# Optimization experiments

Hardware: AMD Instinct MI355X
Metric: run time of the kernel (lower is better)

Reference implementation:

```python
import jax, jax.numpy as jnp
import numpy as np

N_CAMS = 6
N_RAYS = 200
N_UNI = 32
N_G = 4
N_PG = 8
MAX_D = 100.0
SOM_SIG = 2.0
GRID_W = 400
RAW_W, RAW_H = 1600.0, 900.0
SCENE = np.array([-51.2, -51.2, -5.0, 51.2, 51.2, 3.0], dtype=np.float32)
LOSS_W = {'kl': 1.0, 'dist2closest': 0.01, 'color': 1.0, 'reprojection': 1.0}


def _pe(x):
    freqs = jnp.pi * (2.0 ** jnp.arange(6, dtype=x.dtype))
    xb = x[..., None, :] * freqs[:, None]
    flat = lambda t: t.reshape(t.shape[:-2] + (t.shape[-2] * t.shape[-1],))
    return jnp.concatenate([x, flat(jnp.sin(xb)), flat(jnp.cos(xb))], axis=-1)


def _bilinear(img, u, v):
    C, H, W = img.shape
    x0 = jnp.floor(u)
    y0 = jnp.floor(v)
    valid = (u >= 0) & (u <= W - 1) & (v >= 0) & (v <= H - 1)
    x0i = jnp.clip(x0.astype(jnp.int32), 0, W - 1)
    x1i = jnp.clip(x0i + 1, 0, W - 1)
    y0i = jnp.clip(y0.astype(jnp.int32), 0, H - 1)
    y1i = jnp.clip(y0i + 1, 0, H - 1)
    wx = u - x0
    wy = v - y0
    out = (img[:, y0i, x0i] * ((1 - wx) * (1 - wy))[None]
           + img[:, y0i, x1i] * (wx * (1 - wy))[None]
           + img[:, y1i, x0i] * ((1 - wx) * wy)[None]
           + img[:, y1i, x1i] * (wx * wy)[None])
    out = jnp.moveaxis(out, 0, -1) * valid[..., None]
    return out, valid


def _resnet_fc(feat, z, win, bin_, wz, bz, w0, b0, w1, b1, wout, bout):
    x = feat @ win + bin_
    for i in range(wz.shape[0]):
        x = x + z @ wz[i] + bz[i]
        h = jax.nn.relu(x)
        h = jax.nn.relu(h @ w0[i] + b0[i])
        h = h @ w1[i] + b1[i]
        x = x + h
    return jax.nn.relu(x) @ wout + bout


def _forward(cam_feat, bev_feat, source_imgs, target_imgs, raw_cam_Ks, source_cam_Ks,
             lidar2cams, source_cam2input_lidars, source_cam2target_cams,
             mlp_win, mlp_bin, mlp_wz, mlp_bz, mlp_w0, mlp_b0, mlp_w1, mlp_b1, mlp_wout, mlp_bout,
             g_win, g_bin, g_wz, g_bz, g_w0, g_b0, g_w1, g_b1, g_wout, g_bout, pixel_idx):
    cf = cam_feat[0]
    bf = bev_feat[0]
    si = source_imgs[0, 0]
    ti = target_imgs[0, 0]
    rK = raw_cam_Ks[0, :, :3, :3]
    sK = source_cam_Ks[0, 0, :, :3, :3]
    invK = jnp.linalg.inv(sK)
    l2c = lidar2cams[0]
    s2in = source_cam2input_lidars[0, 0]
    s2tg = source_cam2target_cams[0, 0]
    center = jnp.asarray((SCENE[:3] + SCENE[3:]) / 2.0)
    half = jnp.asarray((SCENE[3:] - SCENE[:3]) / 2.0)
    mlp_p = (mlp_win, mlp_bin, mlp_wz, mlp_bz, mlp_w0, mlp_b0, mlp_w1, mlp_b1, mlp_wout, mlp_bout)
    g_p = (g_win, g_bin, g_wz, g_bz, g_w0, g_b0, g_w1, g_b1, g_wout, g_bout)

    def per_cam(cf_c, si_c, ti_c, rK_c, sK_c, invK_c, l2c_c, s2in_c, s2tg_c, idx):
        N = idx.shape[0]
        x = (idx % GRID_W).astype(jnp.float32) * 2.0
        y = (idx // GRID_W).astype(jnp.float32) * 2.0
        pix_h = jnp.stack([x, y, jnp.ones_like(x)], axis=-1)
        dirs = pix_h @ invK_c.T
        d_u = (jnp.arange(N_UNI, dtype=jnp.float32) + 0.5) / N_UNI * MAX_D
        d_u_b = jnp.broadcast_to(d_u, (N, N_UNI))
        Hf, Wf = cf_c.shape[1], cf_c.shape[2]
        Hb, Wb = bf.shape[1], bf.shape[2]

        def eval_pts(d):
            pts_cam = dirs[:, None, :] * d[..., None]
            pts_lid = pts_cam @ s2in_c[:3, :3].T + s2in_c[:3, 3]
            pc = pts_lid @ l2c_c[:3, :3].T + l2c_c[:3, 3]
            z = pc[..., 2]
            zs = jnp.maximum(z, 1e-3)
            uvw = pc @ rK_c.T
            fu = uvw[..., 0] / zs * (Wf / RAW_W)
            fv = uvw[..., 1] / zs * (Hf / RAW_H)
            cam_lat, cval = _bilinear(cf_c, fu, fv)
            cval = cval & (z > 0.1)
            bx = (pts_lid[..., 0] - SCENE[0]) / (SCENE[3] - SCENE[0]) * (Wb - 1)
            by = (pts_lid[..., 1] - SCENE[1]) / (SCENE[4] - SCENE[1]) * (Hb - 1)
            bev_lat, bval = _bilinear(bf, bx, by)
            valid = cval & bval
            latent = jnp.concatenate([bev_lat, cam_lat], axis=-1) * valid[..., None]
            pln = (pts_lid - center) / half
            pcn = pts_cam / MAX_D
            vd = dirs / jnp.linalg.norm(dirs, axis=-1, keepdims=True)
            vdl = vd @ s2in_c[:3, :3].T
            vd_b = jnp.broadcast_to(vd[:, None, :], pcn.shape)
            vdl_b = jnp.broadcast_to(vdl[:, None, :], pcn.shape)
            feat = jnp.concatenate([_pe(pln), vdl_b, _pe(pcn), vd_b], axis=-1)
            return feat, latent, valid

        featc, latc, _valc = eval_pts(d_u_b)
        g = _resnet_fc(featc, latc, *g_p)
        logits = g[..., 0].reshape(N, N_G, N_PG)
        sval = g[..., 1].reshape(N, N_G, N_PG)
        wg = jax.nn.softmax(logits, axis=-1)
        d_grp = d_u.reshape(N_G, N_PG)
        mu = jnp.sum(wg * d_grp, axis=-1)
        std = jax.nn.softplus(jnp.sum(wg * sval, axis=-1)) + 0.1
        offs = jnp.linspace(-2.0, 2.0, N_PG)
        d_g = jnp.clip(mu[..., None] + std[..., None] * offs, 0.5, MAX_D).reshape(N, N_G * N_PG)
        d_all = jnp.sort(jnp.concatenate([d_u_b, d_g], axis=-1), axis=-1)

        featf, latf, valf = eval_pts(d_all)
        out = _resnet_fc(featf, latf, *mlp_p)
        rgb = jax.nn.sigmoid(out[..., :3])
        vf = valf.astype(jnp.float32)
        sigma = jax.nn.softplus(out[..., 3]) * vf
        delta = jnp.concatenate([d_all[..., 1:] - d_all[..., :-1],
                                 jnp.full((N, 1), 1e3, jnp.float32)], axis=-1)
        alpha = 1.0 - jnp.exp(-sigma * delta)
        trans = jnp.cumprod(1.0 - alpha + 1e-10, axis=-1)
        trans = jnp.concatenate([jnp.ones((N, 1), jnp.float32), trans[..., :-1]], axis=-1)
        w = alpha * trans
        color = jnp.sum(w[..., None] * rgb, axis=-2)
        depth = jnp.sum(w * d_all, axis=-1)
        rvr = vf.mean(axis=-1)

        dist2 = (d_all[:, None, :] - mu[:, :, None]) ** 2
        resp = jax.nn.softmax(-dist2 / (2.0 * SOM_SIG ** 2), axis=1)
        rw = resp * w[:, None, :] + 1e-8
        som_mean = jnp.sum(rw * d_all[:, None, :], axis=-1) / jnp.sum(rw, axis=-1)
        som_var = jnp.sum(rw * (d_all[:, None, :] - som_mean[..., None]) ** 2, axis=-1) / jnp.sum(rw, axis=-1)
        som_std = jnp.sqrt(som_var + 1e-6)
        kl = jnp.log(som_std / std) + (std ** 2 + (mu - som_mean) ** 2) / (2.0 * (som_var + 1e-6)) - 0.5
        loss_kl = kl.mean()

        dg = jnp.abs(mu - jax.lax.stop_gradient(depth)[:, None])
        loss_d2c = dg.min(axis=-1).mean()

        csrc, _ = _bilinear(si_c, x, y)
        loss_color = (jnp.abs(csrc - color) * rvr[:, None]).mean()

        pts_c = dirs * depth[:, None]
        pts_t = pts_c @ s2tg_c[:3, :3].T + s2tg_c[:3, 3]
        zt = jnp.maximum(pts_t[..., 2], 1e-3)
        uvt = pts_t @ sK_c.T
        pred, tval = _bilinear(ti_c, uvt[..., 0] / zt, uvt[..., 1] / zt)
        mask = (tval & (pts_t[..., 2] > 0.1) & (depth < 30.0)).astype(jnp.float32)
        l1 = jnp.abs(pred - csrc).mean(axis=-1)
        loss_re = jnp.sum(l1 * mask) / (jnp.sum(mask) + 1e-6)
        return loss_color, loss_kl, loss_d2c, loss_re

    lc, lkl, ld, lr = jax.vmap(per_cam)(cf, si, ti, rK, sK, invK, l2c, s2in, s2tg, pixel_idx)
    lr = jnp.where(jnp.isnan(lr), 0.0, lr)
    denom = float(N_CAMS)
    total = (LOSS_W['color'] * lc.sum() + LOSS_W['kl'] * lkl.sum()
             + LOSS_W['dist2closest'] * ld.sum() + LOSS_W['reprojection'] * lr.sum()) / denom
    return total


def setup_inputs() -> dict:
    key = jax.random.key(0)
    ks = jax.random.split(key, 8)
    f32 = jnp.float32
    cam_feat = jax.random.normal(ks[0], (1, 6, 256, 56, 100), f32)
    bev_feat = jax.random.normal(ks[1], (1, 512, 200, 200), f32)
    source_imgs = jax.random.uniform(ks[2], (1, 1, 6, 3, 300, 800), f32)
    target_imgs = jax.random.uniform(ks[3], (1, 1, 6, 3, 300, 800), f32)
    pixel_idx = jax.random.randint(ks[4], (6, N_RAYS), 0, GRID_W * 150)

    def rz(a):
        c, s = np.cos(a), np.sin(a)
        return np.array([[c, -s, 0.0], [s, c, 0.0], [0.0, 0.0, 1.0]], dtype=np.float32)
    A = np.array([[0, -1, 0], [0, 0, -1], [1, 0, 0]], dtype=np.float32)
    l2c = np.zeros((6, 4, 4), np.float32)
    for i in range(6):
        l2c[i, :3, :3] = A @ rz(-i * np.pi / 3)
        l2c[i, :3, 3] = np.array([0.0, 0.8, 0.5], np.float32)
        l2c[i, 3, 3] = 1.0
    s2in = np.linalg.inv(l2c).astype(np.float32)
    s2in[:, 0, 3] += 0.3
    s2tg = np.tile(np.eye(4, dtype=np.float32), (6, 1, 1))
    ang = 0.03
    s2tg[:, 0, 0] = np.cos(ang); s2tg[:, 0, 2] = np.sin(ang)
    s2tg[:, 2, 0] = -np.sin(ang); s2tg[:, 2, 2] = np.cos(ang)
    s2tg[:, 0, 3] = 0.3; s2tg[:, 2, 3] = 0.1
    rK = np.tile(np.eye(4, dtype=np.float32), (6, 1, 1))
    rK[:, 0, 0] = 800.0; rK[:, 1, 1] = 800.0; rK[:, 0, 2] = 800.0; rK[:, 1, 2] = 450.0
    sKm = np.tile(np.eye(4, dtype=np.float32), (6, 1, 1))
    sKm[:, 0, 0] = 400.0; sKm[:, 1, 1] = 400.0; sKm[:, 0, 2] = 400.0; sKm[:, 1, 2] = 150.0

    D_IN, D_H, D_LAT, NB = 84, 512, 768, 3

    def mk(k, dout):
        kk = jax.random.split(k, 5)
        return dict(
            win=jax.random.normal(kk[0], (D_IN, D_H), f32) * 0.1,
            bin=jnp.zeros((D_H,), f32),
            wz=jax.random.normal(kk[1], (NB, D_LAT, D_H), f32) * 0.036,
            bz=jnp.zeros((NB, D_H), f32),
            w0=jax.random.normal(kk[2], (NB, D_H, D_H), f32) * 0.044,
            b0=jnp.zeros((NB, D_H), f32),
            w1=jax.random.normal(kk[3], (NB, D_H, D_H), f32) * 0.044,
            b1=jnp.zeros((NB, D_H), f32),
            wout=jax.random.normal(kk[4], (D_H, dout), f32) * 0.044,
            bout=jnp.zeros((dout,), f32),
        )
    mp = mk(ks[5], 4)
    gp = mk(ks[6], 2)
    inp = {
        'cam_feat': cam_feat, 'bev_feat': bev_feat,
        'source_imgs': source_imgs, 'target_imgs': target_imgs,
        'raw_cam_Ks': jnp.asarray(rK)[None],
        'source_cam_Ks': jnp.asarray(sKm)[None, None],
        'lidar2cams': jnp.asarray(l2c)[None],
        'source_cam2input_lidars': jnp.asarray(s2in)[None, None],
        'source_cam2target_cams': jnp.asarray(s2tg)[None, None],
        'pixel_idx': pixel_idx,
    }
    for n, v in mp.items():
        inp['mlp_' + n] = v
    for n, v in gp.items():
        inp['g_' + n] = v
    return inp


def reference(cam_feat, bev_feat, source_imgs, target_imgs, raw_cam_Ks, source_cam_Ks,
              lidar2cams, source_cam2input_lidars, source_cam2target_cams,
              mlp_win, mlp_bin, mlp_wz, mlp_bz, mlp_w0, mlp_b0, mlp_w1, mlp_b1, mlp_wout, mlp_bout,
              g_win, g_bin, g_wz, g_bz, g_w0, g_b0, g_w1, g_b1, g_wout, g_bout, pixel_idx):
    return _forward(cam_feat, bev_feat, source_imgs, target_imgs, raw_cam_Ks, source_cam_Ks,
                    lidar2cams, source_cam2input_lidars, source_cam2target_cams,
                    mlp_win, mlp_bin, mlp_wz, mlp_bz, mlp_w0, mlp_b0, mlp_w1, mlp_b1, mlp_wout, mlp_bout,
                    g_win, g_bin, g_wz, g_bz, g_w0, g_b0, g_w1, g_b1, g_wout, g_bout, pixel_idx)
```

## Files before the change

### kernel.cpp

```cpp
#include <hip/hip_runtime.h>
#include <math.h>

typedef unsigned int uint32;
typedef short bf16x8 __attribute__((ext_vector_type(8)));
typedef float f32x4 __attribute__((ext_vector_type(4)));

__device__ __forceinline__ float sigmoidf_(float x){ return 1.0f/(1.0f+expf(-x)); }
__device__ __forceinline__ float softplusf_(float x){ return x>20.0f ? x : log1pf(expf(x)); }
__device__ __forceinline__ int iclampi(int v,int lo,int hi){ return v<lo?lo:(v>hi?hi:v); }

__device__ __forceinline__ float bf2f(uint32 u){ return __uint_as_float(u<<16); }
__device__ __forceinline__ unsigned short f2bf(float f){
  uint32 x = __float_as_uint(f);
  uint32 r = (x + 0x7fffu + ((x>>16)&1u)) >> 16;
  return (unsigned short)r;
}

typedef __attribute__((address_space(1))) const unsigned int ga_u32;
typedef __attribute__((address_space(3))) unsigned int ls_u32;
__device__ __forceinline__ void gl_lds16(const unsigned short* g, unsigned short* l){
  __builtin_amdgcn_global_load_lds((ga_u32*)g, (ls_u32*)l, 16, 0, 0);
}

__device__ __forceinline__ float pe_elem(int s, float vx, float vy, float vz){
  const float F0 = 3.14159265358979f;
  if (s < 3) return s==0?vx:(s==1?vy:vz);
  s -= 3;
  bool isCos = false;
  if (s >= 18){ s -= 18; isCos = true; }
  int fi = s/3, ci = s%3;
  float v = ci==0?vx:(ci==1?vy:vz);
  float f = F0 * (float)(1<<fi);
  return isCos ? cosf(f*v) : sinf(f*v);
}

__global__ __launch_bounds__(256) void transpose_cb_k(const float* __restrict__ in,
    unsigned short* __restrict__ out, int C, int S, int Cout,
    size_t inStride, size_t outStride, int rowStride)
{
  __shared__ float tile[32][33];
  int b = blockIdx.z;
  int s0 = blockIdx.x*32, c0 = blockIdx.y*32;
  int tx = threadIdx.x & 31, ty = threadIdx.x >> 5;
  #pragma unroll
  for (int i=0;i<32;i+=8){
    int c = c0+ty+i, s = s0+tx;
    tile[ty+i][tx] = (c<C && s<S) ? in[(size_t)b*inStride + (size_t)c*S + s] : 0.0f;
  }
  __syncthreads();
  #pragma unroll
  for (int i=0;i<32;i+=8){
    int s = s0+ty+i, c = c0+tx;
    if (s<S && c<Cout) out[(size_t)b*outStride + (size_t)s*rowStride + c] = f2bf(tile[tx][ty+i]);
  }
}

__global__ void combine_bias_k(const float* __restrict__ m_b1, const float* __restrict__ m_bz,
                               const float* __restrict__ g_b1, const float* __restrict__ g_bz,
                               float* __restrict__ CB)
{
  int idx = blockIdx.x*blockDim.x + threadIdx.x;
  if (idx >= 2048) return;
  int w = idx >> 9, n = idx & 511;
  const float* b1 = (w < 2) ? m_b1 : g_b1;
  const float* bz = (w < 2) ? m_bz : g_bz;
  int i = w & 1;
  CB[idx] = b1[i*512 + n] + bz[(i+1)*512 + n];
}

__global__ void setup_rays_k(const int* __restrict__ pix, const float* __restrict__ sK_all,
                             const float* __restrict__ s2in_all,
                             float* __restrict__ dirs, float* __restrict__ vd,
                             float* __restrict__ vdl)
{
  int r = blockIdx.x*blockDim.x + threadIdx.x;
  if (r >= 1200) return;
  int cam = r / 200;
  const float* sK = sK_all + cam*16;
  const float* s2in = s2in_all + cam*16;
  float a=sK[0],b=sK[1],c=sK[2],d=sK[4],e=sK[5],f=sK[6],g=sK[8],h=sK[9],i=sK[10];
  float det = a*(e*i-f*h) - b*(d*i-f*g) + c*(d*h-e*g);
  float inv00=(e*i-f*h)/det, inv01=(c*h-b*i)/det, inv02=(b*f-c*e)/det;
  float inv10=(f*g-d*i)/det, inv11=(a*i-c*g)/det, inv12=(c*d-a*f)/det;
  float inv20=(d*h-e*g)/det, inv21=(b*g-a*h)/det, inv22=(a*e-b*d)/det;
  int idx = pix[r];
  float x = (float)(idx % 400) * 2.0f;
  float y = (float)(idx / 400) * 2.0f;
  float dx = inv00*x + inv01*y + inv02;
  float dy = inv10*x + inv11*y + inv12;
  float dz = inv20*x + inv21*y + inv22;
  dirs[r*3+0]=dx; dirs[r*3+1]=dy; dirs[r*3+2]=dz;
  float n = sqrtf(dx*dx+dy*dy+dz*dz);
  float vx=dx/n, vy=dy/n, vz=dz/n;
  vd[r*3+0]=vx; vd[r*3+1]=vy; vd[r*3+2]=vz;
  vdl[r*3+0]=s2in[0]*vx + s2in[1]*vy + s2in[2]*vz;
  vdl[r*3+1]=s2in[4]*vx + s2in[5]*vy + s2in[6]*vz;
  vdl[r*3+2]=s2in[8]*vx + s2in[9]*vy + s2in[10]*vz;
}

__global__ __launch_bounds__(256) void eval2_k(
    const unsigned short* __restrict__ camT,
    const unsigned short* __restrict__ bevT,
    const float* __restrict__ dirs, const float* __restrict__ vd, const float* __restrict__ vdl,
    const float* __restrict__ dall, int ndepth, int R0,
    const float* __restrict__ s2in_all, const float* __restrict__ l2c_all, const float* __restrict__ rK_all,
    unsigned short* __restrict__ feat, unsigned short* __restrict__ cat, float* __restrict__ vf)
{
  int p  = blockIdx.x;
  int rl = p / ndepth;
  int j  = p - rl*ndepth;
  int R  = R0 + rl;
  int cam = R / 200;
  const float* s2in = s2in_all + cam*16;
  const float* l2c  = l2c_all + cam*16;
  const float* rK   = rK_all + cam*16;
  float dx = dirs[R*3+0], dy = dirs[R*3+1], dz = dirs[R*3+2];
  float d = dall ? dall[(size_t)rl*ndepth + j] : (((float)j + 0.5f)/32.0f)*100.0f;
  float px = dx*d, py = dy*d, pz = dz*d;
  float lx = s2in[0]*px + s2in[1]*py + s2in[2]*pz + s2in[3];
  float ly = s2in[4]*px + s2in[5]*py + s2in[6]*pz + s2in[7];
  float lz = s2in[8]*px + s2in[9]*py + s2in[10]*pz + s2in[11];
  float ccx = l2c[0]*lx + l2c[1]*ly + l2c[2]*lz + l2c[3];
  float ccy = l2c[4]*lx + l2c[5]*ly + l2c[6]*lz + l2c[7];
  float ccz = l2c[8]*lx + l2c[9]*ly + l2c[10]*lz + l2c[11];
  float zs = fmaxf(ccz, 0.001f);
  float uu = rK[0]*ccx + rK[1]*ccy + rK[2]*ccz;
  float vv = rK[4]*ccx + rK[5]*ccy + rK[6]*ccz;
  float fu = uu/zs*(100.0f/1600.0f);
  float fv = vv/zs*(56.0f/900.0f);
  bool cvalid = (fu>=0.0f)&&(fu<=99.0f)&&(fv>=0.0f)&&(fv<=55.0f)&&(ccz>0.1f);
  float cfx0 = floorf(fu), cfy0 = floorf(fv);
  int cx0=iclampi((int)cfx0,0,99), cx1=iclampi(cx0+1,0,99);
  int cy0=iclampi((int)cfy0,0,55), cy1=iclampi(cy0+1,0,55);
  float cwx=fu-cfx0, cwy=fv-cfy0;
  float cw00=(1-cwx)*(1-cwy), cw01=cwx*(1-cwy), cw10=(1-cwx)*cwy, cw11=cwx*cwy;
  float bx = (lx+51.2f)/102.4f*199.0f;
  float by = (ly+51.2f)/102.4f*199.0f;
  bool bvalid = (bx>=0.0f)&&(bx<=199.0f)&&(by>=0.0f)&&(by<=199.0f);
  float bfx0=floorf(bx), bfy0=floorf(by);
  int bx0=iclampi((int)bfx0,0,199), bx1=iclampi(bx0+1,0,199);
  int by0=iclampi((int)bfy0,0,199), by1=iclampi(by0+1,0,199);
  float bwx=bx-bfx0, bwy=by-bfy0;
  float bw00=(1-bwx)*(1-bwy), bw01=bwx*(1-bwy), bw10=(1-bwx)*bwy, bw11=bwx*bwy;
  float vflag = (cvalid && bvalid) ? 1.0f : 0.0f;
  int t = threadIdx.x;
  uint32* catrow = (uint32*)(cat + (size_t)p*1280);
  {
    size_t sb00 = (size_t)(by0*200+bx0)*512, sb01 = (size_t)(by0*200+bx1)*512;
    size_t sb10 = (size_t)(by1*200+bx0)*512, sb11 = (size_t)(by1*200+bx1)*512;
    uint32 u00 = ((const uint32*)(bevT + sb00))[t];
    uint32 u01 = ((const uint32*)(bevT + sb01))[t];
    uint32 u10 = ((const uint32*)(bevT + sb10))[t];
    uint32 u11 = ((const uint32*)(bevT + sb11))[t];
    float lo = bw00*bf2f(u00&0xffffu) + bw01*bf2f(u01&0xffffu) + bw10*bf2f(u10&0xffffu) + bw11*bf2f(u11&0xffffu);
    float hi = bw00*bf2f(u00>>16) + bw01*bf2f(u01>>16) + bw10*bf2f(u10>>16) + bw11*bf2f(u11>>16);
    lo *= vflag; hi *= vflag;
    catrow[256 + t] = (uint32)f2bf(lo) | ((uint32)f2bf(hi)<<16);
  }
  if (t < 128){
    const unsigned short* cfT = camT + (size_t)cam*5600*256;
    size_t sc00 = (size_t)(cy0*100+cx0)*256, sc01 = (size_t)(cy0*100+cx1)*256;
    size_t sc10 = (size_t)(cy1*100+cx0)*256, sc11 = (size_t)(cy1*100+cx1)*256;
    uint32 u00 = ((const uint32*)(cfT + sc00))[t];
    uint32 u01 = ((const uint32*)(cfT + sc01))[t];
    uint32 u10 = ((const uint32*)(cfT + sc10))[t];
    uint32 u11 = ((const uint32*)(cfT + sc11))[t];
    float lo = cw00*bf2f(u00&0xffffu) + cw01*bf2f(u01&0xffffu) + cw10*bf2f(u10&0xffffu) + cw11*bf2f(u11&0xffffu);
    float hi = cw00*bf2f(u00>>16) + cw01*bf2f(u01>>16) + cw10*bf2f(u10>>16) + cw11*bf2f(u11>>16);
    lo *= vflag; hi *= vflag;
    catrow[512 + t] = (uint32)f2bf(lo) | ((uint32)f2bf(hi)<<16);
  }
  if (t < 128){
    float val = 0.0f;
    if (t < 84){
      float plx = lx/51.2f, ply = ly/51.2f, plz = (lz+1.0f)/4.0f;
      float pcx = px/100.0f, pcy = py/100.0f, pcz = pz/100.0f;
      float vx=vd[R*3], vy=vd[R*3+1], vz=vd[R*3+2];
      float wx=vdl[R*3], wy=vdl[R*3+1], wz=vdl[R*3+2];
      if (t < 39)      val = pe_elem(t, plx, ply, plz);
      else if (t < 42) val = (t==39)?wx:((t==40)?wy:wz);
      else if (t < 81) val = pe_elem(t-42, pcx, pcy, pcz);
      else             val = (t==81)?vx:((t==82)?vy:vz);
    }
    feat[(size_t)p*128 + t] = f2bf(val);
  }
  if (vf && t==0) vf[p] = vflag;
}

#define GBM 128
#define GBN 128
#define GBK 64
template<int ACC, int RELU_OUT, int WRITE_XR>
__global__ __launch_bounds__(256) void mgemm_k(
    const unsigned short* __restrict__ A, int lda,
    const unsigned short* __restrict__ BT,
    const float* __restrict__ bias,
    unsigned short* __restrict__ C, int ldc,
    unsigned short* __restrict__ XR,
    int M, int N, int K)
{
  __shared__ unsigned short As[GBM*GBK];
  __shared__ unsigned short Bs[GBN*GBK];
  int w = blockIdx.x;
  int xcd = w & 7, ii = w >> 3;
  int colp = ii & 3, rgrp = ii >> 2;
  int rowp = rgrp*8 + xcd;
  int row0 = rowp*GBM, col0 = colp*GBN;
  if (row0 >= M) return;
  int tid = threadIdx.x;
  int lane = tid & 63, wave = tid >> 6;
  int wm = wave >> 1, wn = wave & 1;
  int l15 = lane & 15, l4 = lane >> 4;
  int lrow = lane >> 3;
  int lch  = lane & 7;
  int chsw = (lch ^ lrow) * 8;
  const unsigned short* aptr = A  + (size_t)(row0 + wave*32 + lrow)*lda + chsw;
  const unsigned short* bptr = BT + (size_t)(col0 + wave*32 + lrow)*K   + chsw;
  unsigned short* asl = &As[(wave*32)*64];
  unsigned short* bsl = &Bs[(wave*32)*64];

  f32x4 acc[4][4];
  #pragma unroll
  for (int mi=0;mi<4;++mi)
    #pragma unroll
    for (int nj=0;nj<4;++nj){ f32x4 z = {0.f,0.f,0.f,0.f}; acc[mi][nj] = z; }

  for (int k0 = 0; k0 < K; k0 += GBK){
    #pragma unroll
    for (int i=0;i<4;++i) gl_lds16(aptr + (size_t)i*8*lda + k0, asl + i*8*64);
    #pragma unroll
    for (int i=0;i<4;++i) gl_lds16(bptr + (size_t)i*8*K   + k0, bsl + i*8*64);
    __syncthreads();
    #pragma unroll
    for (int ks=0; ks<2; ++ks){
      bf16x8 a[4], b[4];
      #pragma unroll
      for (int mi=0;mi<4;++mi){
        int row = wm*64 + mi*16 + l15;
        int sc = (ks*4 + l4) ^ (row&7);
        a[mi] = *(const bf16x8*)&As[row*64 + sc*8];
      }
      #pragma unroll
      for (int nj=0;nj<4;++nj){
        int colr = wn*64 + nj*16 + l15;
        int sc = (ks*4 + l4) ^ (colr&7);
        b[nj] = *(const bf16x8*)&Bs[colr*64 + sc*8];
      }
      #pragma unroll
      for (int mi=0;mi<4;++mi)
        #pragma unroll
        for (int nj=0;nj<4;++nj)
          acc[mi][nj] = __builtin_amdgcn_mfma_f32_16x16x32_bf16(a[mi], b[nj], acc[mi][nj], 0,0,0);
    }
    __syncthreads();
  }
  #pragma unroll
  for (int mi=0;mi<4;++mi){
    int gr0 = row0 + wm*64 + mi*16 + l4*4;
    #pragma unroll
    for (int nj=0;nj<4;++nj){
      int gc = col0 + wn*64 + nj*16 + l15;
      if (gc >= N) continue;
      float bv = bias[gc];
      #pragma unroll
      for (int i=0;i<4;++i){
        int gr = gr0 + i;
        if (gr >= M) continue;
        float v = acc[mi][nj][i] + bv;
        if (ACC) v += bf2f((uint32)C[(size_t)gr*ldc + gc]);
        if (RELU_OUT) v = fmaxf(v, 0.0f);
        C[(size_t)gr*ldc + gc] = f2bf(v);
        if (WRITE_XR) XR[(size_t)gr*512 + gc] = f2bf(fmaxf(v, 0.0f));
      }
    }
  }
}

static inline int gemm_grid(int M){
  int nrow = (M + GBM - 1)/GBM;
  int nrowp = (nrow + 7) & ~7;
  return nrowp * 4;
}

__global__ __launch_bounds__(256) void outlayer_w_k(const unsigned short* __restrict__ X,
    const float* __restrict__ W, const float* __restrict__ b, float* __restrict__ O,
    int M, int dout)
{
  int wid = threadIdx.x >> 6, lane = threadIdx.x & 63;
  int row = blockIdx.x*4 + wid;
  if (row >= M) return;
  const unsigned short* xr = X + (size_t)row*512;
  float s[4] = {0,0,0,0};
  for (int k=lane; k<512; k+=64){
    float xv = fmaxf(bf2f((uint32)xr[k]), 0.0f);
    #pragma unroll
    for (int c=0;c<4;++c)
      if (c < dout) s[c] += xv * W[(size_t)k*dout + c];
  }
  #pragma unroll
  for (int c=0;c<4;++c)
    #pragma unroll
    for (int m=32;m;m>>=1) s[c] += __shfl_xor(s[c], m, 64);
  if (lane == 0)
    for (int c=0;c<dout;++c) O[(size_t)row*dout + c] = s[c] + b[c];
}

__global__ void coarse_post_k(const float* __restrict__ OUTB, float* __restrict__ MU,
                              float* __restrict__ STD, float* __restrict__ DALL,
                              int R0, int rn)
{
  int rl = blockIdx.x*blockDim.x + threadIdx.x;
  if (rl >= rn) return;
  int R = R0 + rl;
  float mu[4], sd[4];
  for (int g=0; g<4; ++g){
    float lg[8], sv[8], mx = -1e30f;
    for (int pp=0; pp<8; ++pp){
      int j = g*8+pp;
      lg[pp] = OUTB[((size_t)rl*32 + j)*2 + 0];
      sv[pp] = OUTB[((size_t)rl*32 + j)*2 + 1];
      mx = fmaxf(mx, lg[pp]);
    }
    float se = 0.0f;
    for (int pp=0; pp<8; ++pp){ lg[pp] = expf(lg[pp]-mx); se += lg[pp]; }
    float m=0.0f, s=0.0f;
    for (int pp=0; pp<8; ++pp){
      float wgt = lg[pp]/se;
      float du = (((float)(g*8+pp)+0.5f)/32.0f)*100.0f;
      m += wgt*du; s += wgt*sv[pp];
    }
    mu[g]=m; sd[g]=softplusf_(s)+0.1f;
    MU[R*4+g]=mu[g]; STD[R*4+g]=sd[g];
  }
  float da[64];
  for (int j=0;j<32;++j) da[j] = (((float)j+0.5f)/32.0f)*100.0f;
  for (int g=0; g<4; ++g)
    for (int pp=0; pp<8; ++pp){
      float off = -2.0f + (4.0f/7.0f)*(float)pp;
      float v = mu[g] + sd[g]*off;
      v = fminf(fmaxf(v, 0.5f), 100.0f);
      da[32 + g*8+pp] = v;
    }
  for (int i=1;i<64;++i){ float key=da[i]; int k=i-1;
    while (k>=0 && da[k]>key){ da[k+1]=da[k]; --k; } da[k+1]=key; }
  for (int j=0;j<64;++j) DALL[(size_t)rl*64+j] = da[j];
}

__device__ __forceinline__ void bilin_img(const float* __restrict__ img, int H, int W,
                                          float u, float v, float* out3, bool* valid)
{
  *valid = (u>=0.0f)&&(u<=(float)(W-1))&&(v>=0.0f)&&(v<=(float)(H-1));
  float fx0=floorf(u), fy0=floorf(v);
  int x0=iclampi((int)fx0,0,W-1), x1=iclampi(x0+1,0,W-1);
  int y0=iclampi((int)fy0,0,H-1), y1=iclampi(y0+1,0,H-1);
  float wx=u-fx0, wy=v-fy0;
  float w00=(1-wx)*(1-wy), w01=wx*(1-wy), w10=(1-wx)*wy, w11=wx*wy;
  for (int ch=0; ch<3; ++ch){
    const float* p = img + (size_t)ch*H*W;
    out3[ch] = w00*p[y0*W+x0] + w01*p[y0*W+x1] + w10*p[y1*W+x0] + w11*p[y1*W+x1];
  }
}

__global__ __launch_bounds__(256) void render_loss_w_k(
  const float* __restrict__ OUTB, const float* __restrict__ VF,
  const float* __restrict__ DALL, const float* __restrict__ MU, const float* __restrict__ STD,
  const float* __restrict__ dirs, const int* __restrict__ pix,
  const float* __restrict__ src_imgs, const float* __restrict__ tgt_imgs,
  const float* __restrict__ s2tg_all, const float* __restrict__ sK_all,
  float* __restrict__ acc, int R0, int rn)
{
  int wid = threadIdx.x >> 6, lane = threadIdx.x & 63;
  int rl = blockIdx.x*4 + wid;
  if (rl >= rn) return;
  int R = R0 + rl;
  int cam = R / 200;
  int j = lane;
  float dj = DALL[(size_t)rl*64 + j];
  float delta = (j<63) ? (DALL[(size_t)rl*64 + j + 1] - dj) : 1000.0f;
  f32x4 o = *(const f32x4*)(OUTB + ((size_t)rl*64 + j)*4);
  float vfp = VF[(size_t)rl*64 + j];
  float sg = softplusf_(o[3])*vfp;
  float alpha = 1.0f - expf(-sg*delta);
  float prod = 1.0f - alpha + 1e-10f;
  #pragma unroll
  for (int dstep=1; dstep<64; dstep<<=1){
    float v = __shfl_up(prod, dstep, 64);
    if (lane >= dstep) prod *= v;
  }
  float T = __shfl_up(prod, 1, 64);
  if (lane == 0) T = 1.0f;
  float w = alpha*T;
  float c0 = w*sigmoidf_(o[0]), c1 = w*sigmoidf_(o[1]), c2 = w*sigmoidf_(o[2]);
  float dsum = w*dj, vs = vfp;
  #pragma unroll
  for (int m=32;m;m>>=1){
    c0 += __shfl_xor(c0,m,64); c1 += __shfl_xor(c1,m,64); c2 += __shfl_xor(c2,m,64);
    dsum += __shfl_xor(dsum,m,64); vs += __shfl_xor(vs,m,64);
  }
// ... 42 lines not shown
  #pragma unroll
  for (int g=0;g<4;++g) mind = fminf(mind, fabsf(mu[g]-depth));
  const float* si = src_imgs + (size_t)cam*3*300*800;
  const float* ti = tgt_imgs + (size_t)cam*3*300*800;
  const float* s2tg = s2tg_all + cam*16;
  const float* sK = sK_all + cam*16;
  int idx = pix[R];
  float x = (float)(idx % 400) * 2.0f;
  float y = (float)(idx / 400) * 2.0f;
  float csrc[3]; bool sval;
  bilin_img(si, 300, 800, x, y, csrc, &sval);
  if (!sval){ csrc[0]=0; csrc[1]=0; csrc[2]=0; }
  float csum = fabsf(csrc[0]-c0)+fabsf(csrc[1]-c1)+fabsf(csrc[2]-c2);
  float dx=dirs[R*3], dy=dirs[R*3+1], dz=dirs[R*3+2];
  float px=dx*depth, py=dy*depth, pz=dz*depth;
  float tx=s2tg[0]*px+s2tg[1]*py+s2tg[2]*pz+s2tg[3];
  float ty=s2tg[4]*px+s2tg[5]*py+s2tg[6]*pz+s2tg[7];
  float tz=s2tg[8]*px+s2tg[9]*py+s2tg[10]*pz+s2tg[11];
  float zt=fmaxf(tz,0.001f);
  float uu=(sK[0]*tx+sK[1]*ty+sK[2]*tz)/zt;
  float vv=(sK[4]*tx+sK[5]*ty+sK[6]*tz)/zt;
  float pred[3]; bool tval;
  bilin_img(ti, 300, 800, uu, vv, pred, &tval);
  float tvf = tval?1.0f:0.0f;
  pred[0]*=tvf; pred[1]*=tvf; pred[2]*=tvf;
  float mask = (tval && (tz>0.1f) && (depth<30.0f)) ? 1.0f : 0.0f;
  float l1 = (fabsf(pred[0]-csrc[0])+fabsf(pred[1]-csrc[1])+fabsf(pred[2]-csrc[2]))*(1.0f/3.0f);
  float* a = acc + cam*8;
  atomicAdd(&a[0], csum*rvr);
  atomicAdd(&a[1], klsum);
  atomicAdd(&a[2], mind);
  atomicAdd(&a[3], l1*mask);
  atomicAdd(&a[4], mask);
}

__global__ void zero_acc_k(float* a){ a[threadIdx.x] = 0.0f; }

__global__ void finalize_k(const float* __restrict__ acc, float* __restrict__ out){
  if (threadIdx.x==0 && blockIdx.x==0){
    float tot = 0.0f;
    for (int c=0;c<6;++c){
      const float* a = acc + c*8;
      float lc  = a[0] / 600.0f;
      float lkl = a[1] / 800.0f;
      float ld  = a[2] / 200.0f;
      float lr  = a[3] / (a[4] + 1e-6f);
      if (lr != lr) lr = 0.0f;
      tot += lc + lkl + 0.01f*ld + lr;
    }
    out[0] = tot / 6.0f;
  }
}

static void run_mlp4(hipStream_t stream, int M,
   const unsigned short* WinT, const float* bin,
   const unsigned short* WzT,  const float* bz,
   const unsigned short* W0T,  const float* b0,
   const unsigned short* W1Wz, const float* CB,
   const unsigned short* W1T2, const float* b1,
   const float* wout, const float* bout, int dout,
   const unsigned short* FEAT, unsigned short* CAT,
   unsigned short* X, unsigned short* XR, float* OUTB)
{
  int g = gemm_grid(M);
  mgemm_k<0,0,1><<<g,256,0,stream>>>(FEAT, 128, WinT, bin, X, 512, XR, M, 512, 128);
  mgemm_k<1,0,1><<<g,256,0,stream>>>(CAT+512, 1280, WzT, bz, X, 512, XR, M, 512, 768);
  for (int i=0;i<2;++i){
    mgemm_k<0,1,0><<<g,256,0,stream>>>(XR, 512, W0T + (size_t)i*512*512, b0 + i*512, CAT, 1280, nullptr, M, 512, 512);
    mgemm_k<1,0,1><<<g,256,0,stream>>>(CAT, 1280, W1Wz + (size_t)i*512*1280, CB + i*512, X, 512, XR, M, 512, 1280);
  }
  mgemm_k<0,1,0><<<g,256,0,stream>>>(XR, 512, W0T + (size_t)2*512*512, b0 + 2*512, CAT, 1280, nullptr, M, 512, 512);
  mgemm_k<1,0,0><<<g,256,0,stream>>>(CAT, 1280, W1T2, b1 + 2*512, X, 512, nullptr, M, 512, 512);
  outlayer_w_k<<<(M+3)/4, 256, 0, stream>>>(X, wout, bout, OUTB, M, dout);
}

extern "C" void kernel_launch(void* const* d_in, const int* in_sizes, int n_in,
                              void* d_out, int out_size, void* d_ws, size_t ws_size,
                              hipStream_t stream) {
  (void)in_sizes; (void)n_in; (void)out_size;
  const float* cam_feat = (const float*)d_in[0];
  const float* bev_feat = (const float*)d_in[1];
  const float* src_imgs = (const float*)d_in[2];
  const float* tgt_imgs = (const float*)d_in[3];
  const float* rK   = (const float*)d_in[4];
  const float* sK   = (const float*)d_in[5];
  const float* l2c  = (const float*)d_in[6];
  const float* s2in = (const float*)d_in[7];
  const float* s2tg = (const float*)d_in[8];
  const int*   pix  = (const int*)d_in[9];
  const float* mlp_win = (const float*)d_in[10];
  const float* mlp_bin = (const float*)d_in[11];
  const float* mlp_wz  = (const float*)d_in[12];
  const float* mlp_bz  = (const float*)d_in[13];
  const float* mlp_w0  = (const float*)d_in[14];
  const float* mlp_b0  = (const float*)d_in[15];
  const float* mlp_w1  = (const float*)d_in[16];
  const float* mlp_b1  = (const float*)d_in[17];
  const float* mlp_wout= (const float*)d_in[18];
  const float* mlp_bout= (const float*)d_in[19];
  const float* g_win = (const float*)d_in[20];
  const float* g_bin = (const float*)d_in[21];
  const float* g_wz  = (const float*)d_in[22];
  const float* g_bz  = (const float*)d_in[23];
  const float* g_w0  = (const float*)d_in[24];
  const float* g_b0  = (const float*)d_in[25];
  const float* g_w1  = (const float*)d_in[26];
  const float* g_b1  = (const float*)d_in[27];
  const float* g_wout= (const float*)d_in[28];
  const float* g_bout= (const float*)d_in[29];

  char* base = (char*)d_ws;
  size_t off = 0;
  auto alloc = [&](size_t bytes)->char*{
    char* p = base + off;
    off = (off + bytes + 255) & ~(size_t)255;
    return p;
  };
  float* ACC  = (float*)alloc(64*4);
  float* DIR  = (float*)alloc(3600*4);
  float* VD   = (float*)alloc(3600*4);
  float* VDL  = (float*)alloc(3600*4);
  float* MU   = (float*)alloc(4800*4);
  float* STD  = (float*)alloc(4800*4);
  float* CBm  = (float*)alloc(2048*4);
  unsigned short* bevT = (unsigned short*)alloc((size_t)40000*512*2);
  unsigned short* camT = (unsigned short*)alloc((size_t)6*5600*256*2);
  unsigned short* gWinT = (unsigned short*)alloc((size_t)512*128*2);
  unsigned short* mWinT = (unsigned short*)alloc((size_t)512*128*2);
  unsigned short* gWzT  = (unsigned short*)alloc((size_t)512*768*2);
  unsigned short* mWzT  = (unsigned short*)alloc((size_t)512*768*2);
  unsigned short* gW0T  = (unsigned short*)alloc((size_t)3*512*512*2);
  unsigned short* mW0T  = (unsigned short*)alloc((size_t)3*512*512*2);
  unsigned short* gW1Wz = (unsigned short*)alloc((size_t)2*512*1280*2);
  unsigned short* mW1Wz = (unsigned short*)alloc((size_t)2*512*1280*2);
  unsigned short* gW1T2 = (unsigned short*)alloc((size_t)512*512*2);
  unsigned short* mW1T2 = (unsigned short*)alloc((size_t)512*512*2);
  size_t fixed = off;
  const size_t perray = 256 + 16384 + 163840 + 65536 + 65536 + 1024 + 256;
  const size_t SLACK = 512*1024;
  int Rc = 1200;
  {
    size_t need = fixed + (size_t)1200*perray + SLACK + 8192;
    if (need > ws_size){
      size_t avail = (ws_size > fixed + SLACK + 8192) ? (ws_size - fixed - SLACK - 8192) : perray;
      Rc = (int)(avail / perray);
      if (Rc < 1) Rc = 1;
      if (Rc > 1200) Rc = 1200;
    }
  }
  float*          DALL = (float*)alloc((size_t)Rc*64*4);
  unsigned short* FEAT = (unsigned short*)alloc((size_t)Rc*64*128*2);
  unsigned short* CAT  = (unsigned short*)alloc((size_t)Rc*64*1280*2);
  unsigned short* X    = (unsigned short*)alloc((size_t)Rc*64*512*2);
  unsigned short* XR   = (unsigned short*)alloc((size_t)Rc*64*512*2);
  float*          OUTB = (float*)alloc((size_t)Rc*64*4*4);
  float*          VF   = (float*)alloc((size_t)Rc*64*4);

  { dim3 g((40000+31)/32, (512+31)/32, 1);
    transpose_cb_k<<<g,256,0,stream>>>(bev_feat, bevT, 512, 40000, 512, 0, 0, 512); }
  { dim3 g((5600+31)/32, (256+31)/32, 6);
    transpose_cb_k<<<g,256,0,stream>>>(cam_feat, camT, 256, 5600, 256, (size_t)256*5600, (size_t)5600*256, 256); }
  { dim3 g((512+31)/32, (128+31)/32, 1);
    transpose_cb_k<<<g,256,0,stream>>>(g_win,  gWinT, 84, 512, 128, 0, 0, 128);
    transpose_cb_k<<<g,256,0,stream>>>(mlp_win, mWinT, 84, 512, 128, 0, 0, 128); }
  { dim3 g((512+31)/32, (768+31)/32, 1);
    transpose_cb_k<<<g,256,0,stream>>>(g_wz,  gWzT, 768, 512, 768, 0, 0, 768);
    transpose_cb_k<<<g,256,0,stream>>>(mlp_wz, mWzT, 768, 512, 768, 0, 0, 768); }
  { dim3 g((512+31)/32, (512+31)/32, 3);
    transpose_cb_k<<<g,256,0,stream>>>(g_w0,  gW0T, 512, 512, 512, (size_t)512*512, (size_t)512*512, 512);
    transpose_cb_k<<<g,256,0,stream>>>(mlp_w0, mW0T, 512, 512, 512, (size_t)512*512, (size_t)512*512, 512); }
  { dim3 g((512+31)/32, (512+31)/32, 2);
    transpose_cb_k<<<g,256,0,stream>>>(g_w1,  gW1Wz, 512, 512, 512, (size_t)512*512, (size_t)512*1280, 1280);
    transpose_cb_k<<<g,256,0,stream>>>(mlp_w1, mW1Wz, 512, 512, 512, (size_t)512*512, (size_t)512*1280, 1280); }
  { dim3 g((512+31)/32, (768+31)/32, 2);
    transpose_cb_k<<<g,256,0,stream>>>(g_wz + (size_t)768*512,  gW1Wz + 512, 768, 512, 768, (size_t)768*512, (size_t)512*1280, 1280);
    transpose_cb_k<<<g,256,0,stream>>>(mlp_wz + (size_t)768*512, mW1Wz + 512, 768, 512, 768, (size_t)768*512, (size_t)512*1280, 1280); }
  { dim3 g((512+31)/32, (512+31)/32, 1);
    transpose_cb_k<<<g,256,0,stream>>>(g_w1 + (size_t)2*512*512,  gW1T2, 512, 512, 512, 0, 0, 512);
    transpose_cb_k<<<g,256,0,stream>>>(mlp_w1 + (size_t)2*512*512, mW1T2, 512, 512, 512, 0, 0, 512); }
  combine_bias_k<<<8,256,0,stream>>>(mlp_b1, mlp_bz, g_b1, g_bz, CBm);

  zero_acc_k<<<1,64,0,stream>>>(ACC);
  setup_rays_k<<<5,256,0,stream>>>(pix, sK, s2in, DIR, VD, VDL);

  for (int R0=0; R0<1200; R0+=Rc){
    int rn = (1200 - R0 < Rc) ? (1200 - R0) : Rc;
    int Pc = rn*32;
    eval2_k<<<Pc,256,0,stream>>>(camT, bevT, DIR, VD, VDL,
        nullptr, 32, R0, s2in, l2c, rK, FEAT, CAT, nullptr);
    run_mlp4(stream, Pc, gWinT,g_bin, gWzT,g_bz, gW0T,g_b0, gW1Wz, CBm+1024,
             gW1T2, g_b1, g_wout, g_bout, 2, FEAT, CAT, X, XR, OUTB);
    coarse_post_k<<<(rn+255)/256,256,0,stream>>>(OUTB, MU, STD, DALL, R0, rn);
    int Pf = rn*64;
    eval2_k<<<Pf,256,0,stream>>>(camT, bevT, DIR, VD, VDL,
        DALL, 64, R0, s2in, l2c, rK, FEAT, CAT, VF);
    run_mlp4(stream, Pf, mWinT,mlp_bin, mWzT,mlp_bz, mW0T,mlp_b0, mW1Wz, CBm,
             mW1T2, mlp_b1, mlp_wout, mlp_bout, 4, FEAT, CAT, X, XR, OUTB);
    render_loss_w_k<<<(rn+3)/4,256,0,stream>>>(OUTB, VF, DALL, MU, STD,
        DIR, pix, src_imgs, tgt_imgs, s2tg, sK, ACC, R0, rn);
  }
  finalize_k<<<1,1,0,stream>>>(ACC, (float*)d_out);
}
```

Baseline: 2.463 ms.

## Fuse input and latent GEMMs, double-buffer GEMM LDS, parallelize coarse post

The positional-encoding features now go straight into an extra slice of the concatenated row buffer, so the input projection (K=128) and the latent projection (K=768) become a single K=896 GEMM with pre-combined biases. This drops one GEMM launch and the separate FEAT buffer per MLP call. The GEMM kernel double-buffers its LDS tiles so the next tile's global-to-LDS load overlaps the MFMAs, removing one barrier per k-step at the cost of twice the shared memory. The per-ray coarse post-processing now runs one wavefront per ray, using shuffle reductions and a rank-based sort in place of a serial per-thread insertion sort.

```diff
diff --git a/kernel.cpp b/kernel.cpp
--- a/kernel.cpp
+++ b/kernel.cpp
@@ -57,15 +57,21 @@
 
 __global__ void combine_bias_k(const float* __restrict__ m_b1, const float* __restrict__ m_bz,
                                const float* __restrict__ g_b1, const float* __restrict__ g_bz,
+                               const float* __restrict__ m_bin, const float* __restrict__ g_bin,
                                float* __restrict__ CB)
 {
   int idx = blockIdx.x*blockDim.x + threadIdx.x;
-  if (idx >= 2048) return;
+  if (idx >= 3072) return;
   int w = idx >> 9, n = idx & 511;
-  const float* b1 = (w < 2) ? m_b1 : g_b1;
-  const float* bz = (w < 2) ? m_bz : g_bz;
-  int i = w & 1;
-  CB[idx] = b1[i*512 + n] + bz[(i+1)*512 + n];
+  float v;
+  if (w < 4){
+    const float* b1 = (w < 2) ? m_b1 : g_b1;
+    const float* bz = (w < 2) ? m_bz : g_bz;
+    int i = w & 1;
+    v = b1[i*512 + n] + bz[(i+1)*512 + n];
+  } else if (w == 4) v = m_bin[n] + m_bz[n];
+  else               v = g_bin[n] + g_bz[n];
+  CB[idx] = v;
 }
 
 __global__ void setup_rays_k(const int* __restrict__ pix, const float* __restrict__ sK_all,
@@ -104,7 +110,7 @@
     const float* __restrict__ dirs, const float* __restrict__ vd, const float* __restrict__ vdl,
     const float* __restrict__ dall, int ndepth, int R0,
     const float* __restrict__ s2in_all, const float* __restrict__ l2c_all, const float* __restrict__ rK_all,
-    unsigned short* __restrict__ feat, unsigned short* __restrict__ cat, float* __restrict__ vf)
+    unsigned short* __restrict__ cat, float* __restrict__ vf)
 {
   int p  = blockIdx.x;
   int rl = p / ndepth;
@@ -144,7 +150,7 @@
   float bw00=(1-bwx)*(1-bwy), bw01=bwx*(1-bwy), bw10=(1-bwx)*bwy, bw11=bwx*bwy;
   float vflag = (cvalid && bvalid) ? 1.0f : 0.0f;
   int t = threadIdx.x;
-  uint32* catrow = (uint32*)(cat + (size_t)p*1280);
+  uint32* catrow = (uint32*)(cat + (size_t)p*1408);
   {
     size_t sb00 = (size_t)(by0*200+bx0)*512, sb01 = (size_t)(by0*200+bx1)*512;
     size_t sb10 = (size_t)(by1*200+bx0)*512, sb11 = (size_t)(by1*200+bx1)*512;
@@ -170,19 +176,20 @@
     lo *= vflag; hi *= vflag;
     catrow[512 + t] = (uint32)f2bf(lo) | ((uint32)f2bf(hi)<<16);
   }
-  if (t < 128){
-    float val = 0.0f;
-    if (t < 84){
-      float plx = lx/51.2f, ply = ly/51.2f, plz = (lz+1.0f)/4.0f;
-      float pcx = px/100.0f, pcy = py/100.0f, pcz = pz/100.0f;
-      float vx=vd[R*3], vy=vd[R*3+1], vz=vd[R*3+2];
-      float wx=vdl[R*3], wy=vdl[R*3+1], wz=vdl[R*3+2];
-      if (t < 39)      val = pe_elem(t, plx, ply, plz);
-      else if (t < 42) val = (t==39)?wx:((t==40)?wy:wz);
-      else if (t < 81) val = pe_elem(t-42, pcx, pcy, pcz);
-      else             val = (t==81)?vx:((t==82)?vy:vz);
-    }
-    feat[(size_t)p*128 + t] = f2bf(val);
+  if (t < 64){
+    float plx = lx/51.2f, ply = ly/51.2f, plz = (lz+1.0f)/4.0f;
+    float pcx = px/100.0f, pcy = py/100.0f, pcz = pz/100.0f;
+    float vx=vd[R*3], vy=vd[R*3+1], vz=vd[R*3+2];
+    float wx=vdl[R*3], wy=vdl[R*3+1], wz=vdl[R*3+2];
+    auto featv = [&](int s)->float{
+      if (s >= 84) return 0.0f;
+      if (s < 39)  return pe_elem(s, plx, ply, plz);
+      if (s < 42)  return (s==39)?wx:((s==40)?wy:wz);
+      if (s < 81)  return pe_elem(s-42, pcx, pcy, pcz);
+      return (s==81)?vx:((s==82)?vy:vz);
+    };
+    float v0 = featv(2*t), v1 = featv(2*t+1);
+    catrow[640 + t] = (uint32)f2bf(v0) | ((uint32)f2bf(v1)<<16);
   }
   if (vf && t==0) vf[p] = vflag;
 }
@@ -199,8 +206,8 @@
     unsigned short* __restrict__ XR,
     int M, int N, int K)
 {
-  __shared__ unsigned short As[GBM*GBK];
-  __shared__ unsigned short Bs[GBN*GBK];
+  __shared__ unsigned short As[2][GBM*GBK];
+  __shared__ unsigned short Bs[2][GBN*GBK];
   int w = blockIdx.x;
   int xcd = w & 7, ii = w >> 3;
   int colp = ii & 3, rgrp = ii >> 2;
@@ -216,8 +223,16 @@
   int chsw = (lch ^ lrow) * 8;
   const unsigned short* aptr = A  + (size_t)(row0 + wave*32 + lrow)*lda + chsw;
   const unsigned short* bptr = BT + (size_t)(col0 + wave*32 + lrow)*K   + chsw;
-  unsigned short* asl = &As[(wave*32)*64];
-  unsigned short* bsl = &Bs[(wave*32)*64];
+  int woff = (wave*32)*64;
+
+  auto STAGE = [&](int buf, int kk){
+    unsigned short* ab = (buf ? &As[1][0] : &As[0][0]) + woff;
+    unsigned short* bb = (buf ? &Bs[1][0] : &Bs[0][0]) + woff;
+    #pragma unroll
+    for (int i=0;i<4;++i) gl_lds16(aptr + (size_t)i*8*lda + kk, ab + i*8*64);
+    #pragma unroll
+    for (int i=0;i<4;++i) gl_lds16(bptr + (size_t)i*8*K   + kk, bb + i*8*64);
+  };
 
   f32x4 acc[4][4];
   #pragma unroll
@@ -225,12 +240,13 @@
     #pragma unroll
     for (int nj=0;nj<4;++nj){ f32x4 z = {0.f,0.f,0.f,0.f}; acc[mi][nj] = z; }
 
-  for (int k0 = 0; k0 < K; k0 += GBK){
-    #pragma unroll
-    for (int i=0;i<4;++i) gl_lds16(aptr + (size_t)i*8*lda + k0, asl + i*8*64);
-    #pragma unroll
-    for (int i=0;i<4;++i) gl_lds16(bptr + (size_t)i*8*K   + k0, bsl + i*8*64);
+  STAGE(0, 0);
+  int nk = K / GBK;
+  for (int t=0; t<nk; ++t){
     __syncthreads();
+    if (t+1 < nk) STAGE((t+1)&1, (t+1)*GBK);
+    const unsigned short* Ab = (t&1) ? &As[1][0] : &As[0][0];
+    const unsigned short* Bb = (t&1) ? &Bs[1][0] : &Bs[0][0];
     #pragma unroll
     for (int ks=0; ks<2; ++ks){
       bf16x8 a[4], b[4];
@@ -238,13 +254,13 @@
       for (int mi=0;mi<4;++mi){
         int row = wm*64 + mi*16 + l15;
         int sc = (ks*4 + l4) ^ (row&7);
-        a[mi] = *(const bf16x8*)&As[row*64 + sc*8];
+        a[mi] = *(const bf16x8*)&Ab[row*64 + sc*8];
       }
       #pragma unroll
       for (int nj=0;nj<4;++nj){
         int colr = wn*64 + nj*16 + l15;
         int sc = (ks*4 + l4) ^ (colr&7);
-        b[nj] = *(const bf16x8*)&Bs[colr*64 + sc*8];
+        b[nj] = *(const bf16x8*)&Bb[colr*64 + sc*8];
       }
       #pragma unroll
       for (int mi=0;mi<4;++mi)
@@ -252,7 +268,6 @@
         for (int nj=0;nj<4;++nj)
           acc[mi][nj] = __builtin_amdgcn_mfma_f32_16x16x32_bf16(a[mi], b[nj], acc[mi][nj], 0,0,0);
     }
-    __syncthreads();
   }
   #pragma unroll
   for (int mi=0;mi<4;++mi){
@@ -305,45 +320,54 @@
     for (int c=0;c<dout;++c) O[(size_t)row*dout + c] = s[c] + b[c];
 }
 
-__global__ void coarse_post_k(const float* __restrict__ OUTB, float* __restrict__ MU,
-                              float* __restrict__ STD, float* __restrict__ DALL,
-                              int R0, int rn)
-{
-  int rl = blockIdx.x*blockDim.x + threadIdx.x;
+__global__ __launch_bounds__(256) void coarse_post_w_k(const float* __restrict__ OUTB,
+    float* __restrict__ MU, float* __restrict__ STD, float* __restrict__ DALL,
+    int R0, int rn)
+{
+  int wid = threadIdx.x >> 6, lane = threadIdx.x & 63;
+  int rl = blockIdx.x*4 + wid;
   if (rl >= rn) return;
   int R = R0 + rl;
-  float mu[4], sd[4];
-  for (int g=0; g<4; ++g){
-    float lg[8], sv[8], mx = -1e30f;
-    for (int pp=0; pp<8; ++pp){
-      int j = g*8+pp;
-      lg[pp] = OUTB[((size_t)rl*32 + j)*2 + 0];
-      sv[pp] = OUTB[((size_t)rl*32 + j)*2 + 1];
-      mx = fmaxf(mx, lg[pp]);
+  float v = 0.0f, muv = 0.0f, sdv = 0.0f;
+  if (lane < 32){
+    float lg = OUTB[((size_t)rl*32 + lane)*2 + 0];
+    float sv = OUTB[((size_t)rl*32 + lane)*2 + 1];
+    float mx = lg;
+    #pragma unroll
+    for (int m=1;m<8;m<<=1) mx = fmaxf(mx, __shfl_xor(mx, m, 64));
+    float e = expf(lg - mx);
+    float se = e;
+    #pragma unroll
+    for (int m=1;m<8;m<<=1) se += __shfl_xor(se, m, 64);
+    float du = ((float)lane + 0.5f)/32.0f*100.0f;
+    float wgt = e/se;
+    float mp = wgt*du, sp = wgt*sv;
+    #pragma unroll
+    for (int m=1;m<8;m<<=1){ mp += __shfl_xor(mp, m, 64); sp += __shfl_xor(sp, m, 64); }
+    muv = mp; sdv = softplusf_(sp) + 0.1f;
+    if ((lane & 7) == 0){
+      MU[R*4 + (lane>>3)] = muv;
+      STD[R*4 + (lane>>3)] = sdv;
     }
-    float se = 0.0f;
-    for (int pp=0; pp<8; ++pp){ lg[pp] = expf(lg[pp]-mx); se += lg[pp]; }
-    float m=0.0f, s=0.0f;
-    for (int pp=0; pp<8; ++pp){
-      float wgt = lg[pp]/se;
-      float du = (((float)(g*8+pp)+0.5f)/32.0f)*100.0f;
-      m += wgt*du; s += wgt*sv[pp];
+    v = du;
+  }
+  {
+    int g = (lane - 32) >> 3;
+    int src = (lane >= 32) ? g*8 : 0;
+    float mub = __shfl(muv, src, 64);
+    float sdb = __shfl(sdv, src, 64);
+    if (lane >= 32){
+      int pp = (lane - 32) & 7;
+      float off = -2.0f + (4.0f/7.0f)*(float)pp;
+      v = fminf(fmaxf(mub + sdb*off, 0.5f), 100.0f);
     }
-    mu[g]=m; sd[g]=softplusf_(s)+0.1f;
-    MU[R*4+g]=mu[g]; STD[R*4+g]=sd[g];
-  }
-  float da[64];
-  for (int j=0;j<32;++j) da[j] = (((float)j+0.5f)/32.0f)*100.0f;
-  for (int g=0; g<4; ++g)
-    for (int pp=0; pp<8; ++pp){
-      float off = -2.0f + (4.0f/7.0f)*(float)pp;
-      float v = mu[g] + sd[g]*off;
-      v = fminf(fmaxf(v, 0.5f), 100.0f);
-      da[32 + g*8+pp] = v;
-    }
-  for (int i=1;i<64;++i){ float key=da[i]; int k=i-1;
-    while (k>=0 && da[k]>key){ da[k+1]=da[k]; --k; } da[k+1]=key; }
-  for (int j=0;j<64;++j) DALL[(size_t)rl*64+j] = da[j];
+  }
+  int rank = 0;
+  for (int i=0;i<64;++i){
+    float vi = __shfl(v, i, 64);
+    rank += (vi < v) || (vi == v && i < lane);
+  }
+  DALL[(size_t)rl*64 + rank] = v;
 }
 
 __device__ __forceinline__ void bilin_img(const float* __restrict__ img, int H, int W,
@@ -492,25 +516,22 @@
   }
 }
 
-static void run_mlp4(hipStream_t stream, int M,
-   const unsigned short* WinT, const float* bin,
-   const unsigned short* WzT,  const float* bz,
-   const unsigned short* W0T,  const float* b0,
+static void run_mlp5(hipStream_t stream, int M,
+   const unsigned short* WmT, const float* CBin,
+   const unsigned short* W0T, const float* b0,
    const unsigned short* W1Wz, const float* CB,
    const unsigned short* W1T2, const float* b1,
    const float* wout, const float* bout, int dout,
-   const unsigned short* FEAT, unsigned short* CAT,
-   unsigned short* X, unsigned short* XR, float* OUTB)
+   unsigned short* CAT, unsigned short* X, unsigned short* XR, float* OUTB)
 {
   int g = gemm_grid(M);
-  mgemm_k<0,0,1><<<g,256,0,stream>>>(FEAT, 128, WinT, bin, X, 512, XR, M, 512, 128);
-  mgemm_k<1,0,1><<<g,256,0,stream>>>(CAT+512, 1280, WzT, bz, X, 512, XR, M, 512, 768);
+  mgemm_k<0,0,1><<<g,256,0,stream>>>(CAT+512, 1408, WmT, CBin, X, 512, XR, M, 512, 896);
   for (int i=0;i<2;++i){
-    mgemm_k<0,1,0><<<g,256,0,stream>>>(XR, 512, W0T + (size_t)i*512*512, b0 + i*512, CAT, 1280, nullptr, M, 512, 512);
-    mgemm_k<1,0,1><<<g,256,0,stream>>>(CAT, 1280, W1Wz + (size_t)i*512*1280, CB + i*512, X, 512, XR, M, 512, 1280);
-  }
-  mgemm_k<0,1,0><<<g,256,0,stream>>>(XR, 512, W0T + (size_t)2*512*512, b0 + 2*512, CAT, 1280, nullptr, M, 512, 512);
-  mgemm_k<1,0,0><<<g,256,0,stream>>>(CAT, 1280, W1T2, b1 + 2*512, X, 512, nullptr, M, 512, 512);
+    mgemm_k<0,1,0><<<g,256,0,stream>>>(XR, 512, W0T + (size_t)i*512*512, b0 + i*512, CAT, 1408, nullptr, M, 512, 512);
+    mgemm_k<1,0,1><<<g,256,0,stream>>>(CAT, 1408, W1Wz + (size_t)i*512*1280, CB + i*512, X, 512, XR, M, 512, 1280);
+  }
+  mgemm_k<0,1,0><<<g,256,0,stream>>>(XR, 512, W0T + (size_t)2*512*512, b0 + 2*512, CAT, 1408, nullptr, M, 512, 512);
+  mgemm_k<1,0,0><<<g,256,0,stream>>>(CAT, 1408, W1T2, b1 + 2*512, X, 512, nullptr, M, 512, 512);
   outlayer_w_k<<<(M+3)/4, 256, 0, stream>>>(X, wout, bout, OUTB, M, dout);
 }
 
@@ -562,13 +583,11 @@
   float* VDL  = (float*)alloc(3600*4);
   float* MU   = (float*)alloc(4800*4);
   float* STD  = (float*)alloc(4800*4);
-  float* CBm  = (float*)alloc(2048*4);
+  float* CBm  = (float*)alloc(3072*4);
   unsigned short* bevT = (unsigned short*)alloc((size_t)40000*512*2);
   unsigned short* camT = (unsigned short*)alloc((size_t)6*5600*256*2);
-  unsigned short* gWinT = (unsigned short*)alloc((size_t)512*128*2);
-  unsigned short* mWinT = (unsigned short*)alloc((size_t)512*128*2);
-  unsigned short* gWzT  = (unsigned short*)alloc((size_t)512*768*2);
-  unsigned short* mWzT  = (unsigned short*)alloc((size_t)512*768*2);
+  unsigned short* gWmT  = (unsigned short*)alloc((size_t)512*896*2);
+  unsigned short* mWmT  = (unsigned short*)alloc((size_t)512*896*2);
   unsigned short* gW0T  = (unsigned short*)alloc((size_t)3*512*512*2);
   unsigned short* mW0T  = (unsigned short*)alloc((size_t)3*512*512*2);
   unsigned short* gW1Wz = (unsigned short*)alloc((size_t)2*512*1280*2);
@@ -576,7 +595,7 @@
   unsigned short* gW1T2 = (unsigned short*)alloc((size_t)512*512*2);
   unsigned short* mW1T2 = (unsigned short*)alloc((size_t)512*512*2);
   size_t fixed = off;
-  const size_t perray = 256 + 16384 + 163840 + 65536 + 65536 + 1024 + 256;
+  const size_t perray = 256 + 180224 + 65536 + 65536 + 1024 + 256;
   const size_t SLACK = 512*1024;
   int Rc = 1200;
   {
@@ -584,13 +603,13 @@
     if (need > ws_size){
       size_t avail = (ws_size > fixed + SLACK + 8192) ? (ws_size - fixed - SLACK - 8192) : perray;
       Rc = (int)(avail / perray);
-      if (Rc < 1) Rc = 1;
+      if (Rc < 2) Rc = 2;
+      Rc &= ~1;
       if (Rc > 1200) Rc = 1200;
     }
   }
   float*          DALL = (float*)alloc((size_t)Rc*64*4);
-  unsigned short* FEAT = (unsigned short*)alloc((size_t)Rc*64*128*2);
-  unsigned short* CAT  = (unsigned short*)alloc((size_t)Rc*64*1280*2);
+  unsigned short* CAT  = (unsigned short*)alloc((size_t)Rc*64*1408*2);
   unsigned short* X    = (unsigned short*)alloc((size_t)Rc*64*512*2);
   unsigned short* XR   = (unsigned short*)alloc((size_t)Rc*64*512*2);
   float*          OUTB = (float*)alloc((size_t)Rc*64*4*4);
@@ -600,12 +619,12 @@
     transpose_cb_k<<<g,256,0,stream>>>(bev_feat, bevT, 512, 40000, 512, 0, 0, 512); }
   { dim3 g((5600+31)/32, (256+31)/32, 6);
     transpose_cb_k<<<g,256,0,stream>>>(cam_feat, camT, 256, 5600, 256, (size_t)256*5600, (size_t)5600*256, 256); }
+  { dim3 g((512+31)/32, (768+31)/32, 1);
+    transpose_cb_k<<<g,256,0,stream>>>(g_wz,  gWmT, 768, 512, 768, 0, 0, 896);
+    transpose_cb_k<<<g,256,0,stream>>>(mlp_wz, mWmT, 768, 512, 768, 0, 0, 896); }
   { dim3 g((512+31)/32, (128+31)/32, 1);
-    transpose_cb_k<<<g,256,0,stream>>>(g_win,  gWinT, 84, 512, 128, 0, 0, 128);
-    transpose_cb_k<<<g,256,0,stream>>>(mlp_win, mWinT, 84, 512, 128, 0, 0, 128); }
-  { dim3 g((512+31)/32, (768+31)/32, 1);
-    transpose_cb_k<<<g,256,0,stream>>>(g_wz,  gWzT, 768, 512, 768, 0, 0, 768);
-    transpose_cb_k<<<g,256,0,stream>>>(mlp_wz, mWzT, 768, 512, 768, 0, 0, 768); }
+    transpose_cb_k<<<g,256,0,stream>>>(g_win,  gWmT+768, 84, 512, 128, 0, 0, 896);
+    transpose_cb_k<<<g,256,0,stream>>>(mlp_win, mWmT+768, 84, 512, 128, 0, 0, 896); }
   { dim3 g((512+31)/32, (512+31)/32, 3);
     transpose_cb_k<<<g,256,0,stream>>>(g_w0,  gW0T, 512, 512, 512, (size_t)512*512, (size_t)512*512, 512);
     transpose_cb_k<<<g,256,0,stream>>>(mlp_w0, mW0T, 512, 512, 512, (size_t)512*512, (size_t)512*512, 512); }
@@ -618,7 +637,7 @@
   { dim3 g((512+31)/32, (512+31)/32, 1);
     transpose_cb_k<<<g,256,0,stream>>>(g_w1 + (size_t)2*512*512,  gW1T2, 512, 512, 512, 0, 0, 512);
     transpose_cb_k<<<g,256,0,stream>>>(mlp_w1 + (size_t)2*512*512, mW1T2, 512, 512, 512, 0, 0, 512); }
-  combine_bias_k<<<8,256,0,stream>>>(mlp_b1, mlp_bz, g_b1, g_bz, CBm);
+  combine_bias_k<<<12,256,0,stream>>>(mlp_b1, mlp_bz, g_b1, g_bz, mlp_bin, g_bin, CBm);
 
   zero_acc_k<<<1,64,0,stream>>>(ACC);
   setup_rays_k<<<5,256,0,stream>>>(pix, sK, s2in, DIR, VD, VDL);
@@ -627,15 +646,15 @@
     int rn = (1200 - R0 < Rc) ? (1200 - R0) : Rc;
     int Pc = rn*32;
     eval2_k<<<Pc,256,0,stream>>>(camT, bevT, DIR, VD, VDL,
-        nullptr, 32, R0, s2in, l2c, rK, FEAT, CAT, nullptr);
-    run_mlp4(stream, Pc, gWinT,g_bin, gWzT,g_bz, gW0T,g_b0, gW1Wz, CBm+1024,
-             gW1T2, g_b1, g_wout, g_bout, 2, FEAT, CAT, X, XR, OUTB);
-    coarse_post_k<<<(rn+255)/256,256,0,stream>>>(OUTB, MU, STD, DALL, R0, rn);
+        nullptr, 32, R0, s2in, l2c, rK, CAT, nullptr);
+    run_mlp5(stream, Pc, gWmT, CBm+2560, gW0T, g_b0, gW1Wz, CBm+1024,
+             gW1T2, g_b1, g_wout, g_bout, 2, CAT, X, XR, OUTB);
+    coarse_post_w_k<<<(rn+3)/4,256,0,stream>>>(OUTB, MU, STD, DALL, R0, rn);
     int Pf = rn*64;
     eval2_k<<<Pf,256,0,stream>>>(camT, bevT, DIR, VD, VDL,
-        DALL, 64, R0, s2in, l2c, rK, FEAT, CAT, VF);
-    run_mlp4(stream, Pf, mWinT,mlp_bin, mWzT,mlp_bz, mW0T,mlp_b0, mW1Wz, CBm,
-             mW1T2, mlp_b1, mlp_wout, mlp_bout, 4, FEAT, CAT, X, XR, OUTB);
+        DALL, 64, R0, s2in, l2c, rK, CAT, VF);
+    run_mlp5(stream, Pf, mWmT, CBm+2048, mW0T, mlp_b0, mW1Wz, CBm,
+             mW1T2, mlp_b1, mlp_wout, mlp_bout, 4, CAT, X, XR, OUTB);
     render_loss_w_k<<<(rn+3)/4,256,0,stream>>>(OUTB, VF, DALL, MU, STD,
         DIR, pix, src_imgs, tgt_imgs, s2tg, sK, ACC, R0, rn);
   }
```

Result: faster. 2.121 ms (-13.9%).
